# Kernel optimization log

Measured on AMD Instinct MI355X. Metric: run time of the kernel, lower is better.

The kernel has to match this reference:

```python
import jax, jax.numpy as jnp
import numpy as np

D = 1024      # input_dim
H = 1024      # expert_hidden_dim
O = 1024      # output_dim
E = 8         # num_experts
TOPK = 2
B, N_OBJ = 4, 4096


def setup_inputs() -> dict:
    key = jax.random.key(0)
    ks = jax.random.split(key, 7)
    s_in = 1.0 / np.sqrt(D)
    s_h = 1.0 / np.sqrt(H)
    return {
        "x":  jax.random.normal(ks[0], (B, N_OBJ, D), dtype=jnp.float32),
        "Wr": jax.random.uniform(ks[1], (D, E), jnp.float32, -s_in, s_in),
        "br": jax.random.uniform(ks[2], (E,), jnp.float32, -s_in, s_in),
        "W1": jax.random.uniform(ks[3], (E, D, H), jnp.float32, -s_in, s_in),
        "b1": jax.random.uniform(ks[4], (E, H), jnp.float32, -s_in, s_in),
        "W2": jax.random.uniform(ks[5], (E, H, O), jnp.float32, -s_h, s_h),
        "b2": jax.random.uniform(ks[6], (E, O), jnp.float32, -s_h, s_h),
    }


def reference(x, Wr, br, W1, b1, W2, b2):
    # Router: (B, N, E)
    logits = jnp.einsum("bnd,de->bne", x, Wr) + br
    # sparse top-k routing: softmax over the top-k logits only
    topv, topi = jax.lax.top_k(logits, TOPK)          # (B, N, k)
    coef = jax.nn.softmax(topv, axis=-1)              # (B, N, k)
    # scatter per-expert coefficients into dense (B, N, E); zeros for non-selected
    coef_full = jnp.sum(
        jax.nn.one_hot(topi, E, dtype=x.dtype) * coef[..., None], axis=-2
    )                                                 # (B, N, E)
    # All-expert dense compute (as in original module; dropout is eval-mode identity)
    h = jax.nn.relu(jnp.einsum("bnd,edh->benh", x, W1) + b1[:, None, :])  # (B,E,N,H)
    y = jnp.einsum("benh,eho->beno", h, W2) + b2[:, None, :]              # (B,E,N,O)
    # Weighted combine over experts
    out = jnp.einsum("beno,bne->bno", y, coef_full)                        # (B,N,O)
    return out
```

## Files before the change

### kernel.cpp

```cpp
#include <hip/hip_runtime.h>
#include <cstdint>

typedef unsigned short u16;
using bf16x8 = __attribute__((ext_vector_type(8))) __bf16;
using f32x4  = __attribute__((ext_vector_type(4))) float;
typedef u16 u16x8 __attribute__((ext_vector_type(8)));

#define T_TOK 16384
#define E_NUM 8

__device__ __forceinline__ u16 f2bf(float f) {
    union { float f; unsigned u; } v; v.f = f;
    unsigned r = (v.u + 0x7FFFu + ((v.u >> 16) & 1u)) >> 16;
    return (u16)r;
}

__device__ __forceinline__ void gload_lds16(const void* g, void* l) {
    __builtin_amdgcn_global_load_lds(
        (const __attribute__((address_space(1))) void*)g,
        (__attribute__((address_space(3))) void*)l, 16, 0, 0);
}

__global__ __launch_bounds__(256) void k_transpose(const float* __restrict__ W, u16* __restrict__ WT) {
    __shared__ float tile[32][33];
    int e = blockIdx.z;
    int d0 = blockIdx.x << 5, h0 = blockIdx.y << 5;
    int tx = threadIdx.x & 31, ty = threadIdx.x >> 5;
    const size_t eo = (size_t)e << 20;
#pragma unroll
    for (int i = 0; i < 4; ++i) {
        int r = ty + i * 8;
        tile[r][tx] = W[eo + (size_t)(d0 + r) * 1024 + h0 + tx];
    }
    __syncthreads();
#pragma unroll
    for (int i = 0; i < 4; ++i) {
        int r = ty + i * 8;
        WT[eo + (size_t)(h0 + r) * 1024 + d0 + tx] = f2bf(tile[tx][r]);
    }
}

__global__ __launch_bounds__(256) void k_router(const float* __restrict__ x, const float* __restrict__ Wr,
                                                const float* __restrict__ br,
                                                int* __restrict__ tinfo, float* __restrict__ c1arr,
                                                u16* __restrict__ xbf) {
    const int wave = threadIdx.x >> 6, lane = threadIdx.x & 63;
    const int t = (blockIdx.x << 2) + wave;
    const float* xr = x + (size_t)t * 1024;
    u16* xbr = xbf + (size_t)t * 1024;
    float acc[8] = {0, 0, 0, 0, 0, 0, 0, 0};
#pragma unroll
    for (int i = 0; i < 16; ++i) {
        int d = (i << 6) + lane;
        float xv = xr[d];
        xbr[d] = f2bf(xv);
        float4 w0 = *(const float4*)(Wr + d * 8);
        float4 w1 = *(const float4*)(Wr + d * 8 + 4);
        acc[0] += xv * w0.x; acc[1] += xv * w0.y; acc[2] += xv * w0.z; acc[3] += xv * w0.w;
        acc[4] += xv * w1.x; acc[5] += xv * w1.y; acc[6] += xv * w1.z; acc[7] += xv * w1.w;
    }
#pragma unroll
    for (int off = 32; off > 0; off >>= 1)
#pragma unroll
        for (int e = 0; e < 8; ++e) acc[e] += __shfl_xor(acc[e], off);

    if (lane == 0) {
        float v1 = -1e30f, v2 = -1e30f; int i1 = 0, i2 = 0;
#pragma unroll
        for (int e = 0; e < 8; ++e) {
            float v = acc[e] + br[e];
            if (v > v1) { v2 = v1; i2 = i1; v1 = v; i1 = e; }
            else if (v > v2) { v2 = v; i2 = e; }
        }
        float c1 = 1.f / (1.f + expf(v2 - v1));
        tinfo[t] = i1 | (i2 << 4);
        c1arr[t] = c1;
    }
}

__global__ __launch_bounds__(1024) void k_scatter(const int* __restrict__ tinfo, const float* __restrict__ c1arr,
                                                  int* __restrict__ cnt, int* __restrict__ tok,
                                                  float* __restrict__ coef) {
    __shared__ int lcnt[8];
    __shared__ int lbase[8];
    const int tid = threadIdx.x;
    const int t = blockIdx.x * 1024 + tid;
    if (tid < 8) lcnt[tid] = 0;
    __syncthreads();
    int info = tinfo[t];
    float c1 = c1arr[t];
    int g1 = info & 15;
    int g2 = (info >> 4) & 15;
    int o1 = atomicAdd(&lcnt[g1], 1);
    int o2 = atomicAdd(&lcnt[g2], 1);
    __syncthreads();
    if (tid < 8) lbase[tid] = atomicAdd(cnt + tid, lcnt[tid]);
    __syncthreads();
    int p1 = lbase[g1] + o1;
    tok[(g1 << 14) + p1] = t; coef[(g1 << 14) + p1] = c1;
    int p2 = lbase[g2] + o2;
    tok[(g2 << 14) + p2] = t; coef[(g2 << 14) + p2] = 1.f - c1;
}

template <int PHASE>
__global__ __launch_bounds__(256, 2) void k_gemm(
    const int* __restrict__ cnt, const int* __restrict__ tok, const float* __restrict__ coef,
    const u16* __restrict__ xbf, const u16* __restrict__ w1t, const u16* __restrict__ w2t,
    const float* __restrict__ b1, const float* __restrict__ b2,
    u16* __restrict__ hbuf, float* __restrict__ out)
{
    __shared__ u16 a0_s[128 * 64];
    __shared__ u16 a1_s[128 * 64];
    __shared__ u16 b0_s[128 * 64];
    __shared__ u16 b1_s[128 * 64];
    __shared__ int s_cnt[8];
    __shared__ int tok_s[128];
    __shared__ float coef_s[128];

    const int tid = threadIdx.x;
    if (tid < 8) s_cnt[tid] = cnt[tid];
    __syncthreads();

    int bid = blockIdx.x + blockIdx.y * 264;
    int lin = (bid & 7) * 264 + (bid >> 3);
    int xt = lin >> 3, yt = lin & 7;

    int g = -1, tile = 0, r0 = 0, mt = xt, rb = 0;
    for (int gg = 0; gg < 8; ++gg) {
        int c = s_cnt[gg], tg = (c + 127) >> 7;
        if (g < 0) {
            if (mt < tg) { g = gg; tile = mt; r0 = rb + (mt << 7); }
            else mt -= tg;
        }
        rb += c;
    }
    if (g < 0) return;
    const int cntg = s_cnt[g];
    const int e = g;
    const int nb = yt << 7;
    const int rowlim = cntg - (tile << 7);

    if (tid < 128) {
        int idx = (tile << 7) + tid;
        bool valid = idx < cntg;
        tok_s[tid] = valid ? tok[(g << 14) + idx] : 0;
        coef_s[tid] = valid ? coef[(g << 14) + idx] : 0.f;
    }
    __syncthreads();

    const int w = tid >> 6, l = tid & 63;
    const int wrow = (w >> 1) << 6, wcol = (w & 1) << 6;
    const u16* asrc = (PHASE == 0) ? xbf : hbuf;
    const u16* bsrc = (PHASE == 0) ? w1t : w2t;
    const size_t brow0 = ((size_t)e << 10) + nb;

    const int sw = ((l & 7) ^ (l >> 3)) << 3;
    const int xk = (l & 7) << 3;

    const u16* aptr[4]; int ldsa[4];
#pragma unroll
    for (int j = 0; j < 4; ++j) {
        int row = (j << 5) + (w << 3) + (l >> 3);
        int arow = (PHASE == 0) ? tok_s[row] : (r0 + row);
        aptr[j] = asrc + ((size_t)arow << 10) + sw;
        ldsa[j] = ((j << 5) + (w << 3)) * 64;
    }
    const u16* bptr[4]; int ldsb[4];
#pragma unroll
    for (int j = 0; j < 4; ++j) {
        int brow = (j << 5) + (w << 3) + (l >> 3);
        bptr[j] = bsrc + (brow0 + brow) * 1024 + sw;
        ldsb[j] = ((j << 5) + (w << 3)) * 64;
    }

    f32x4 acc[4][4];
#pragma unroll
    for (int mi = 0; mi < 4; ++mi)
#pragma unroll
        for (int ni = 0; ni < 4; ++ni) { acc[mi][ni][0] = 0.f; acc[mi][ni][1] = 0.f; acc[mi][ni][2] = 0.f; acc[mi][ni][3] = 0.f; }

#define STAGE(AS, BS, KO)                                                     \
    {                                                                         \
        _Pragma("unroll")                                                     \
        for (int j = 0; j < 4; ++j) gload_lds16(aptr[j] + (KO), &AS[ldsa[j]]); \
        _Pragma("unroll")                                                     \
        for (int j = 0; j < 4; ++j) gload_lds16(bptr[j] + (KO), &BS[ldsb[j]]); \
    }

#define COMPUTE(AS, BS)                                                       \
    {                                                                         \
        _Pragma("unroll")                                                     \
        for (int ks = 0; ks < 64; ks += 32) {                                 \
            const int co = (ks + ((l >> 4) << 3)) ^ xk;                       \
            bf16x8 af[4], bfr[4];                                             \
            _Pragma("unroll")                                                 \
            for (int mi = 0; mi < 4; ++mi)                                    \
                af[mi] = *(const bf16x8*)&AS[(wrow + (mi << 4) + (l & 15)) * 64 + co]; \
            _Pragma("unroll")                                                 \
            for (int ni = 0; ni < 4; ++ni)                                    \
                bfr[ni] = *(const bf16x8*)&BS[(wcol + (ni << 4) + (l & 15)) * 64 + co]; \
            _Pragma("unroll")                                                 \
            for (int mi = 0; mi < 4; ++mi)                                    \
                _Pragma("unroll")                                             \
                for (int ni = 0; ni < 4; ++ni)                                \
                    acc[mi][ni] = __builtin_amdgcn_mfma_f32_16x16x32_bf16(af[mi], bfr[ni], acc[mi][ni], 0, 0, 0); \
        }                                                                     \
    }

    STAGE(a0_s, b0_s, 0);
    __syncthreads();

    for (int kc = 0; kc < 16; kc += 2) {
        if (kc + 1 < 16) STAGE(a1_s, b1_s, (kc + 1) << 6);
        COMPUTE(a0_s, b0_s);
        __syncthreads();
        if (kc + 2 < 16) STAGE(a0_s, b0_s, (kc + 2) << 6);
        COMPUTE(a1_s, b1_s);
        __syncthreads();
    }
#undef STAGE
#undef COMPUTE

    const int rq = (l >> 4) << 2;
    const int cl = l & 15;
#pragma unroll
    for (int ni = 0; ni < 4; ++ni) {
        int ccol = wcol + (ni << 4) + cl;
        float bias = (PHASE == 0 ? b1 : b2)[((size_t)e << 10) + nb + ccol];
#pragma unroll
        for (int mi = 0; mi < 4; ++mi) {
            int rbase = wrow + (mi << 4) + rq;
#pragma unroll
            for (int j = 0; j < 4; ++j) {
                int r = rbase + j;
                if (r < rowlim) {
                    float v = acc[mi][ni][j] + bias;
                    if constexpr (PHASE == 0) {
                        v = fmaxf(v, 0.f);
                        hbuf[(size_t)(r0 + r) * 1024 + nb + ccol] = f2bf(v);
                    } else {
                        atomicAdd(out + ((size_t)tok_s[r] << 10) + nb + ccol, v * coef_s[r]);
                    }
                }
            }
        }
    }
}

__global__ __launch_bounds__(256) void k_naive(const float* __restrict__ x, const float* __restrict__ Wr,
    const float* __restrict__ br, const float* __restrict__ W1, const float* __restrict__ b1,
    const float* __restrict__ W2, const float* __restrict__ b2, float* __restrict__ out)
{
    __shared__ float xs[1024];
    __shared__ float hs[1024];
    __shared__ float red[4];
    __shared__ float lg[8];
    const int tid = threadIdx.x;
    const size_t t = blockIdx.x;
    for (int i = tid; i < 1024; i += 256) xs[i] = x[t * 1024 + i];
    __syncthreads();
    float lacc[8] = {0, 0, 0, 0, 0, 0, 0, 0};
    for (int d = tid; d < 1024; d += 256) {
        float xv = xs[d];
#pragma unroll
        for (int e = 0; e < 8; ++e) lacc[e] += xv * Wr[d * 8 + e];
    }
    for (int e = 0; e < 8; ++e) {
        float v = lacc[e];
        for (int off = 32; off > 0; off >>= 1) v += __shfl_xor(v, off);
        if ((tid & 63) == 0) red[tid >> 6] = v;
        __syncthreads();
        if (tid == 0) lg[e] = red[0] + red[1] + red[2] + red[3] + br[e];
        __syncthreads();
    }
    float v1 = -1e30f, v2 = -1e30f; int i1 = 0, i2 = 0;
    for (int e = 0; e < 8; ++e) {
        float v = lg[e];
        if (v > v1) { v2 = v1; i2 = i1; v1 = v; i1 = e; }
        else if (v > v2) { v2 = v; i2 = e; }
    }
    float c1 = 1.f / (1.f + expf(v2 - v1)), c2 = 1.f - c1;
    float yacc[4] = {0, 0, 0, 0};
    for (int slot = 0; slot < 2; ++slot) {
        int e = slot ? i2 : i1;
        float cw = slot ? c2 : c1;
        __syncthreads();
        float ha[4];
        for (int jb = 0; jb < 4; ++jb) {
            int j = (jb << 8) + tid;
            float a = b1[(e << 10) + j];
            for (int d = 0; d < 1024; ++d) a += xs[d] * W1[(((size_t)e << 10) + d) * 1024 + j];
            ha[jb] = fmaxf(a, 0.f);
        }
        for (int jb = 0; jb < 4; ++jb) hs[(jb << 8) + tid] = ha[jb];
        __syncthreads();
        for (int ob = 0; ob < 4; ++ob) {
            int o = (ob << 8) + tid;
            float a = b2[(e << 10) + o];
            for (int h = 0; h < 1024; ++h) a += hs[h] * W2[(((size_t)e << 10) + h) * 1024 + o];
            yacc[ob] += cw * a;
        }
    }
    for (int ob = 0; ob < 4; ++ob) out[t * 1024 + (ob << 8) + tid] = yacc[ob];
}

extern "C" void kernel_launch(void* const* d_in, const int* in_sizes, int n_in,
                              void* d_out, int out_size, void* d_ws, size_t ws_size,
                              hipStream_t stream) {
    const float* x  = (const float*)d_in[0];
    const float* Wr = (const float*)d_in[1];
    const float* br = (const float*)d_in[2];
    const float* W1 = (const float*)d_in[3];
    const float* b1 = (const float*)d_in[4];
    const float* W2 = (const float*)d_in[5];
    const float* b2 = (const float*)d_in[6];
    float* out = (float*)d_out;

    const size_t OFF_TOK   = (size_t)1 << 20;
    const size_t OFF_COEF  = (size_t)2 << 20;
    const size_t OFF_TINFO = (size_t)3 << 20;
    const size_t OFF_C1    = OFF_TINFO + (size_t)T_TOK * 4;
    const size_t OFF_XBF   = (size_t)4 << 20;
    const size_t OFF_W1T   = OFF_XBF + (size_t)T_TOK * 1024 * 2;
    const size_t OFF_W2T   = OFF_W1T + (size_t)E_NUM * 1024 * 1024 * 2;
    const size_t OFF_H     = OFF_W2T + (size_t)E_NUM * 1024 * 1024 * 2;
    const size_t WS_NEED   = OFF_H + (size_t)(2 * T_TOK + 512) * 1024 * 2;

    if (ws_size < WS_NEED) {
        k_naive<<<T_TOK, 256, 0, stream>>>(x, Wr, br, W1, b1, W2, b2, out);
        return;
    }

    char* ws = (char*)d_ws;
    int*   cnt   = (int*)ws;
    int*   tok   = (int*)(ws + OFF_TOK);
    float* coef  = (float*)(ws + OFF_COEF);
    int*   tinfo = (int*)(ws + OFF_TINFO);
    float* c1arr = (float*)(ws + OFF_C1);
    u16*   xbf   = (u16*)(ws + OFF_XBF);
    u16*   w1t   = (u16*)(ws + OFF_W1T);
    u16*   w2t   = (u16*)(ws + OFF_W2T);
    u16*   hbuf  = (u16*)(ws + OFF_H);

    hipMemsetAsync(cnt, 0, 64, stream);
    hipMemsetAsync(d_out, 0, (size_t)out_size * sizeof(float), stream);
    k_transpose<<<dim3(32, 32, 8), 256, 0, stream>>>(W1, w1t);
    k_transpose<<<dim3(32, 32, 8), 256, 0, stream>>>(W2, w2t);
    k_router<<<4096, 256, 0, stream>>>(x, Wr, br, tinfo, c1arr, xbf);
    k_scatter<<<16, 1024, 0, stream>>>(tinfo, c1arr, cnt, tok, coef);
    dim3 gg(264, 8);
    k_gemm<0><<<gg, 256, 0, stream>>>(cnt, tok, coef, xbf, w1t, w2t, b1, b2, hbuf, out);
    k_gemm<1><<<gg, 256, 0, stream>>>(cnt, tok, coef, xbf, w1t, w2t, b1, b2, hbuf, out);
}
```

Measured before the change: 431.1 us.

## Shrink GEMM N-tile to 64 and pipeline loads with explicit waitcnt barriers

Halves the output-column tile of the grouped expert GEMM from 128 to 64, which doubles the grid and cuts LDS and accumulator use so three blocks can reside per CU. The K loop is restructured to prefetch two stages ahead, using raw s_waitcnt vmcnt/lgkmcnt plus s_barrier instead of __syncthreads, so global-to-LDS loads overlap compute more tightly. The cost is lower arithmetic intensity per tile: each A tile is reloaded twice as often and the MFMA-to-LDS-read ratio per wave drops.

```diff
diff --git a/kernel.cpp b/kernel.cpp
--- a/kernel.cpp
+++ b/kernel.cpp
@@ -4,7 +4,6 @@
 typedef unsigned short u16;
 using bf16x8 = __attribute__((ext_vector_type(8))) __bf16;
 using f32x4  = __attribute__((ext_vector_type(4))) float;
-typedef u16 u16x8 __attribute__((ext_vector_type(8)));
 
 #define T_TOK 16384
 #define E_NUM 8
@@ -103,7 +102,7 @@
 }
 
 template <int PHASE>
-__global__ __launch_bounds__(256, 2) void k_gemm(
+__global__ __launch_bounds__(256, 3) void k_gemm(
     const int* __restrict__ cnt, const int* __restrict__ tok, const float* __restrict__ coef,
     const u16* __restrict__ xbf, const u16* __restrict__ w1t, const u16* __restrict__ w2t,
     const float* __restrict__ b1, const float* __restrict__ b2,
@@ -111,8 +110,8 @@
 {
     __shared__ u16 a0_s[128 * 64];
     __shared__ u16 a1_s[128 * 64];
-    __shared__ u16 b0_s[128 * 64];
-    __shared__ u16 b1_s[128 * 64];
+    __shared__ u16 b0_s[64 * 64];
+    __shared__ u16 b1_s[64 * 64];
     __shared__ int s_cnt[8];
     __shared__ int tok_s[128];
     __shared__ float coef_s[128];
@@ -121,9 +120,9 @@
     if (tid < 8) s_cnt[tid] = cnt[tid];
     __syncthreads();
 
-    int bid = blockIdx.x + blockIdx.y * 264;
-    int lin = (bid & 7) * 264 + (bid >> 3);
-    int xt = lin >> 3, yt = lin & 7;
+    int bid = blockIdx.x + blockIdx.y * 272;
+    int lin = (bid & 7) * 544 + (bid >> 3);
+    int xt = lin >> 4, yt = lin & 15;
 
     int g = -1, tile = 0, r0 = 0, mt = xt, rb = 0;
     for (int gg = 0; gg < 8; ++gg) {
@@ -137,7 +136,7 @@
     if (g < 0) return;
     const int cntg = s_cnt[g];
     const int e = g;
-    const int nb = yt << 7;
+    const int nb = yt << 6;
     const int rowlim = cntg - (tile << 7);
 
     if (tid < 128) {
@@ -149,7 +148,7 @@
     __syncthreads();
 
     const int w = tid >> 6, l = tid & 63;
-    const int wrow = (w >> 1) << 6, wcol = (w & 1) << 6;
+    const int wrow = (w >> 1) << 6, wcol = (w & 1) << 5;
     const u16* asrc = (PHASE == 0) ? xbf : hbuf;
     const u16* bsrc = (PHASE == 0) ? w1t : w2t;
     const size_t brow0 = ((size_t)e << 10) + nb;
@@ -165,66 +164,91 @@
         aptr[j] = asrc + ((size_t)arow << 10) + sw;
         ldsa[j] = ((j << 5) + (w << 3)) * 64;
     }
-    const u16* bptr[4]; int ldsb[4];
-#pragma unroll
-    for (int j = 0; j < 4; ++j) {
+    const u16* bptr[2]; int ldsb[2];
+#pragma unroll
+    for (int j = 0; j < 2; ++j) {
         int brow = (j << 5) + (w << 3) + (l >> 3);
         bptr[j] = bsrc + (brow0 + brow) * 1024 + sw;
         ldsb[j] = ((j << 5) + (w << 3)) * 64;
     }
 
-    f32x4 acc[4][4];
+    f32x4 acc[4][2];
 #pragma unroll
     for (int mi = 0; mi < 4; ++mi)
 #pragma unroll
-        for (int ni = 0; ni < 4; ++ni) { acc[mi][ni][0] = 0.f; acc[mi][ni][1] = 0.f; acc[mi][ni][2] = 0.f; acc[mi][ni][3] = 0.f; }
-
-#define STAGE(AS, BS, KO)                                                     \
-    {                                                                         \
-        _Pragma("unroll")                                                     \
+        for (int ni = 0; ni < 2; ++ni) { acc[mi][ni][0] = 0.f; acc[mi][ni][1] = 0.f; acc[mi][ni][2] = 0.f; acc[mi][ni][3] = 0.f; }
+
+#define STAGE(AS, BS, KO)                                                      \
+    {                                                                          \
+        _Pragma("unroll")                                                      \
         for (int j = 0; j < 4; ++j) gload_lds16(aptr[j] + (KO), &AS[ldsa[j]]); \
-        _Pragma("unroll")                                                     \
-        for (int j = 0; j < 4; ++j) gload_lds16(bptr[j] + (KO), &BS[ldsb[j]]); \
-    }
-
-#define COMPUTE(AS, BS)                                                       \
-    {                                                                         \
-        _Pragma("unroll")                                                     \
-        for (int ks = 0; ks < 64; ks += 32) {                                 \
-            const int co = (ks + ((l >> 4) << 3)) ^ xk;                       \
-            bf16x8 af[4], bfr[4];                                             \
-            _Pragma("unroll")                                                 \
-            for (int mi = 0; mi < 4; ++mi)                                    \
+        _Pragma("unroll")                                                      \
+        for (int j = 0; j < 2; ++j) gload_lds16(bptr[j] + (KO), &BS[ldsb[j]]); \
+    }
+
+#define COMPUTE(AS, BS)                                                        \
+    {                                                                          \
+        _Pragma("unroll")                                                      \
+        for (int ks = 0; ks < 64; ks += 32) {                                  \
+            const int co = (ks + ((l >> 4) << 3)) ^ xk;                        \
+            bf16x8 af[4], bfr[2];                                              \
+            _Pragma("unroll")                                                  \
+            for (int mi = 0; mi < 4; ++mi)                                     \
                 af[mi] = *(const bf16x8*)&AS[(wrow + (mi << 4) + (l & 15)) * 64 + co]; \
-            _Pragma("unroll")                                                 \
-            for (int ni = 0; ni < 4; ++ni)                                    \
+            _Pragma("unroll")                                                  \
+            for (int ni = 0; ni < 2; ++ni)                                     \
                 bfr[ni] = *(const bf16x8*)&BS[(wcol + (ni << 4) + (l & 15)) * 64 + co]; \
-            _Pragma("unroll")                                                 \
-            for (int mi = 0; mi < 4; ++mi)                                    \
-                _Pragma("unroll")                                             \
-                for (int ni = 0; ni < 4; ++ni)                                \
+            _Pragma("unroll")                                                  \
+            for (int mi = 0; mi < 4; ++mi)                                     \
+                _Pragma("unroll")                                              \
+                for (int ni = 0; ni < 2; ++ni)                                 \
                     acc[mi][ni] = __builtin_amdgcn_mfma_f32_16x16x32_bf16(af[mi], bfr[ni], acc[mi][ni], 0, 0, 0); \
-        }                                                                     \
-    }
+        }                                                                      \
+    }
+
+#define VM6  asm volatile("s_waitcnt vmcnt(6)" ::: "memory")
+#define VM0  asm volatile("s_waitcnt vmcnt(0)" ::: "memory")
+#define LGK0 asm volatile("s_waitcnt lgkmcnt(0)" ::: "memory")
+#define BAR() { asm volatile("" ::: "memory"); __builtin_amdgcn_s_barrier(); asm volatile("" ::: "memory"); }
 
     STAGE(a0_s, b0_s, 0);
-    __syncthreads();
-
-    for (int kc = 0; kc < 16; kc += 2) {
-        if (kc + 1 < 16) STAGE(a1_s, b1_s, (kc + 1) << 6);
+    STAGE(a1_s, b1_s, 64);
+    VM6; BAR();
+
+    for (int kc = 0; kc < 12; kc += 2) {
         COMPUTE(a0_s, b0_s);
-        __syncthreads();
-        if (kc + 2 < 16) STAGE(a0_s, b0_s, (kc + 2) << 6);
+        LGK0; BAR();
+        STAGE(a0_s, b0_s, (kc + 2) << 6);
+        VM6; BAR();
         COMPUTE(a1_s, b1_s);
-        __syncthreads();
-    }
+        LGK0; BAR();
+        STAGE(a1_s, b1_s, (kc + 3) << 6);
+        VM6; BAR();
+    }
+    COMPUTE(a0_s, b0_s);
+    LGK0; BAR();
+    STAGE(a0_s, b0_s, 14 << 6);
+    VM6; BAR();
+    COMPUTE(a1_s, b1_s);
+    LGK0; BAR();
+    STAGE(a1_s, b1_s, 15 << 6);
+    VM6; BAR();
+    COMPUTE(a0_s, b0_s);
+    LGK0; BAR();
+    VM0; BAR();
+    COMPUTE(a1_s, b1_s);
+
 #undef STAGE
 #undef COMPUTE
+#undef VM6
+#undef VM0
+#undef LGK0
+#undef BAR
 
     const int rq = (l >> 4) << 2;
     const int cl = l & 15;
 #pragma unroll
-    for (int ni = 0; ni < 4; ++ni) {
+    for (int ni = 0; ni < 2; ++ni) {
         int ccol = wcol + (ni << 4) + cl;
         float bias = (PHASE == 0 ? b1 : b2)[((size_t)e << 10) + nb + ccol];
 #pragma unroll
@@ -348,7 +372,7 @@
     k_transpose<<<dim3(32, 32, 8), 256, 0, stream>>>(W2, w2t);
     k_router<<<4096, 256, 0, stream>>>(x, Wr, br, tinfo, c1arr, xbf);
     k_scatter<<<16, 1024, 0, stream>>>(tinfo, c1arr, cnt, tok, coef);
-    dim3 gg(264, 8);
+    dim3 gg(272, 16);
     k_gemm<0><<<gg, 256, 0, stream>>>(cnt, tok, coef, xbf, w1t, w2t, b1, b2, hbuf, out);
     k_gemm<1><<<gg, 256, 0, stream>>>(cnt, tok, coef, xbf, w1t, w2t, b1, b2, hbuf, out);
 }
```

New measurement: 393.1 us. 1.1x faster.
